# Kernel optimization log

Hardware: AMD Instinct MI355X
Metric: run time of the kernel (lower is better)

The kernel has to match this reference:

```python
import jax, jax.numpy as jnp
import numpy as np

VOCAB, EMB, H, T, B, S = 30000, 300, 512, 9, 128, 256


def setup_inputs() -> dict:
    key = jax.random.key(0)
    ks = jax.random.split(key, 16)
    sc = 0.1
    inp = {
        "inputs": jax.random.randint(ks[0], (B, S), 0, VOCAB, dtype=jnp.int32),
        "tags": jax.random.randint(ks[1], (B, S), 0, T, dtype=jnp.int32),
        "masks": jnp.ones((B, S), dtype=bool),
        "emb": jax.random.normal(ks[2], (VOCAB, EMB), jnp.float32),
        "w_ih_f": jax.random.normal(ks[3], (4 * H, EMB), jnp.float32) * sc,
        "w_hh_f": jax.random.normal(ks[4], (4 * H, H), jnp.float32) * sc,
        "b_f": jax.random.normal(ks[5], (4 * H,), jnp.float32) * sc,
        "w_ih_b": jax.random.normal(ks[6], (4 * H, EMB), jnp.float32) * sc,
        "w_hh_b": jax.random.normal(ks[7], (4 * H, H), jnp.float32) * sc,
        "b_b": jax.random.normal(ks[8], (4 * H,), jnp.float32) * sc,
        "fc_w": jax.random.normal(ks[9], (T, 2 * H), jnp.float32) * sc,
        "trans": jax.random.normal(ks[10], (T, T), jnp.float32) * sc,
        "start_trans": jax.random.normal(ks[11], (T,), jnp.float32) * sc,
        "end_trans": jax.random.normal(ks[12], (T,), jnp.float32) * sc,
    }
    return inp


def _run_lstm(x, w_ih, w_hh, b, reverse):
    # x: (B,S,E); pytorch gate order i,f,g,o; b = b_ih + b_hh combined
    xg = jnp.einsum('bse,ge->bsg', x, w_ih) + b  # (B,S,4H)
    if reverse:
        xg = xg[:, ::-1]
    h0 = jnp.zeros((x.shape[0], w_hh.shape[1]), x.dtype)

    def step(carry, xt):
        h, c = carry
        g = xt + h @ w_hh.T
        i, f, gg, o = jnp.split(g, 4, axis=-1)
        c = jax.nn.sigmoid(f) * c + jax.nn.sigmoid(i) * jnp.tanh(gg)
        h = jax.nn.sigmoid(o) * jnp.tanh(c)
        return (h, c), h

    _, hs = jax.lax.scan(step, (h0, h0), xg.transpose(1, 0, 2))
    hs = hs.transpose(1, 0, 2)  # (B,S,H)
    if reverse:
        hs = hs[:, ::-1]
    return hs


def _crf_llh(emissions, tags, masks, trans, start_trans, end_trans):
    # torchcrf log-likelihood, reduction='sum'
    Bn, Sn, Tn = emissions.shape
    mf = masks.astype(emissions.dtype)
    bidx = jnp.arange(Bn)
    first = tags[:, 0]
    num = start_trans[first] + emissions[bidx, 0, first]
    prev, cur = tags[:, :-1], tags[:, 1:]
    step_sc = trans[prev, cur] + jnp.take_along_axis(emissions[:, 1:], cur[..., None], -1)[..., 0]
    num = num + jnp.sum(step_sc * mf[:, 1:], axis=1)
    seq_ends = masks.sum(1) - 1
    last = tags[bidx, seq_ends]
    num = num + end_trans[last]

    score0 = start_trans + emissions[:, 0]  # (B,T)

    def step(score, xs):
        em_t, m_t = xs  # (B,T), (B,)
        nxt = jax.nn.logsumexp(score[:, :, None] + trans[None] + em_t[:, None, :], axis=1)
        score = jnp.where(m_t[:, None], nxt, score)
        return score, None

    score, _ = jax.lax.scan(step, score0,
                            (emissions[:, 1:].transpose(1, 0, 2), masks[:, 1:].T))
    logZ = jax.nn.logsumexp(score + end_trans, axis=1)
    return jnp.sum(num - logZ)


def reference(inputs, tags, masks, emb, w_ih_f, w_hh_f, b_f, w_ih_b, w_hh_b, b_b,
              fc_w, trans, start_trans, end_trans):
    x = emb[inputs]  # (B,S,E); dropout is identity at eval
    hf = _run_lstm(x, w_ih_f, w_hh_f, b_f, reverse=False)
    hb = _run_lstm(x, w_ih_b, w_hh_b, b_b, reverse=True)
    feats = jnp.concatenate([hf, hb], axis=-1)  # (B,S,2H)
    emissions = jnp.einsum('bsh,th->bst', feats, fc_w)
    return _crf_llh(emissions, tags, masks, trans, start_trans, end_trans)
```

## Files before the change

### kernel.cpp

```cpp
#include <hip/hip_runtime.h>
#include <hip/hip_bf16.h>
#include <stdint.h>

#define B_    128
#define S_    256
#define T_    9

typedef __bf16 bf16;
typedef bf16  bf16x8 __attribute__((ext_vector_type(8)));
typedef bf16  bf16x4 __attribute__((ext_vector_type(4)));
typedef float f32x4  __attribute__((ext_vector_type(4)));
typedef unsigned long long u64;

__device__ __forceinline__ float sigm(float x)  { return 1.f / (1.f + __expf(-x)); }
__device__ __forceinline__ float tanhx(float x) { return 2.f / (1.f + __expf(-2.f * x)) - 1.f; }

#define SBlg() do { asm volatile("s_waitcnt lgkmcnt(0)" ::: "memory"); \
                    __builtin_amdgcn_s_barrier(); } while (0)

__global__ void prep_kernel(const float* __restrict__ wihf, const float* __restrict__ whhf,
                            const float* __restrict__ bf_,  const float* __restrict__ wihb,
                            const float* __restrict__ whhb, const float* __restrict__ bb_,
                            bf16* __restrict__ wih_r, bf16* __restrict__ whh_r,
                            float* __restrict__ bias_r)
{
    int64_t idx = (int64_t)blockIdx.x * blockDim.x + threadIdx.x;
    const int64_t N1 = 2LL * 2048 * 320;
    const int64_t N2 = 2LL * 2048 * 512;
    const int64_t N3 = 4096;
    if (idx < N1) {
        int k = (int)(idx % 320);
        int64_t r = idx / 320;
        int row = (int)(r % 2048), dir = (int)(r / 2048);
        const float* w = dir ? wihb : wihf;
        int orig = (row & 3) * 512 + (row >> 2);
        float v = (k < 300) ? w[(int64_t)orig * 300 + k] : 0.f;
        wih_r[idx] = (bf16)v;
    } else if (idx < N1 + N2) {
        int64_t i = idx - N1;
        int k = (int)(i % 512);
        int64_t r = i / 512;
        int row = (int)(r % 2048), dir = (int)(r / 2048);
        const float* w = dir ? whhb : whhf;
        int orig = (row & 3) * 512 + (row >> 2);
        int x = k & 31;
        int ks = (x & 16) | (((x >> 1) & 1) << 3) | ((x & 1) << 2)
               | (((x >> 3) & 1) << 1) | ((x >> 2) & 1);
        int ksrc = (k & ~31) | ks;
        whh_r[i] = (bf16)w[(int64_t)orig * 512 + ksrc];
    } else if (idx < N1 + N2 + N3) {
        int i = (int)(idx - (N1 + N2));
        int row = i & 2047, dir = i >> 11;
        const float* bb = dir ? bb_ : bf_;
        int orig = (row & 3) * 512 + (row >> 2);
        bias_r[i] = bb[orig];
    }
}

__global__ __launch_bounds__(256, 1) void fused_lstm_kernel(
    const int* __restrict__ inputs, const float* __restrict__ emb,
    const bf16* __restrict__ wih_r, const bf16* __restrict__ whh_r,
    const float* __restrict__ bias_r, const float* __restrict__ fcw,
    u64* __restrict__ hbuf, float* __restrict__ em_part)
{
    const int bid = blockIdx.x;
    const int gid = bid & 15;
    const int gslice = bid >> 4;
    const int dir = gid >> 3, bs = gid & 7;
    const int tid = threadIdx.x;
    const int w = tid >> 6, lane = tid & 63;
    const int l15 = lane & 15, l4 = lane >> 4;

    __shared__ __align__(16) char h_s[16384];
    __shared__ __align__(16) char ring[16384];
    __shared__ __align__(16) char x_s[20480];
    __shared__ __align__(16) bf16 h_sm[2 * 16 * 32];
    __shared__ float em_lds[2][2][144];

    auto load_h = [&](int t) {
        const u64 wt = (u64)t;
        const u64 want = (wt << 16) | (wt << 48);
        const u64 MSK  = 0xffff0000ffff0000ull;
        const u64* base = hbuf + ((size_t)(((t & 1) * 2 + dir) * 8 + bs) * 16) * 256 + tid;
        const u64* p0 = base;        const u64* p1 = base + 512;
        const u64* p2 = base + 1024; const u64* p3 = base + 1536;
        const u64* p4 = base + 2048; const u64* p5 = base + 2560;
        const u64* p6 = base + 3072; const u64* p7 = base + 3584;
        u64 v[16];
        asm volatile(
            "global_load_dwordx2 %0, %16, off sc1\n\t"
            "global_load_dwordx2 %1, %16, off offset:2048 sc1\n\t"
            "global_load_dwordx2 %2, %17, off sc1\n\t"
            "global_load_dwordx2 %3, %17, off offset:2048 sc1\n\t"
            "global_load_dwordx2 %4, %18, off sc1\n\t"
            "global_load_dwordx2 %5, %18, off offset:2048 sc1\n\t"
            "global_load_dwordx2 %6, %19, off sc1\n\t"
            "global_load_dwordx2 %7, %19, off offset:2048 sc1\n\t"
            "global_load_dwordx2 %8, %20, off sc1\n\t"
            "global_load_dwordx2 %9, %20, off offset:2048 sc1\n\t"
            "global_load_dwordx2 %10, %21, off sc1\n\t"
            "global_load_dwordx2 %11, %21, off offset:2048 sc1\n\t"
            "global_load_dwordx2 %12, %22, off sc1\n\t"
            "global_load_dwordx2 %13, %22, off offset:2048 sc1\n\t"
            "global_load_dwordx2 %14, %23, off sc1\n\t"
            "global_load_dwordx2 %15, %23, off offset:2048 sc1\n\t"
            "s_waitcnt vmcnt(0)"
            : "=&v"(v[0]), "=&v"(v[1]), "=&v"(v[2]), "=&v"(v[3]),
              "=&v"(v[4]), "=&v"(v[5]), "=&v"(v[6]), "=&v"(v[7]),
              "=&v"(v[8]), "=&v"(v[9]), "=&v"(v[10]), "=&v"(v[11]),
              "=&v"(v[12]), "=&v"(v[13]), "=&v"(v[14]), "=&v"(v[15])
            : "v"(p0), "v"(p1), "v"(p2), "v"(p3),
              "v"(p4), "v"(p5), "v"(p6), "v"(p7)
            : "memory");
        __builtin_amdgcn_sched_barrier(0);
        int rounds = 0;
        while (true) {
            unsigned wst = 0;
#pragma unroll
            for (int g = 0; g < 16; ++g)
                if (__any((int)((v[g] & MSK) != want))) wst |= (1u << g);
            if (wst == 0) break;
            if (++rounds > (1 << 14)) break;
            if (rounds > 1) __builtin_amdgcn_s_sleep(1);
#pragma unroll
            for (int g = 0; g < 16; ++g)
                if (wst & (1u << g))
                    asm volatile("global_load_dwordx2 %0, %1, off sc1"
                                 : "=v"(v[g]) : "v"(base + g * 256) : "memory");
            asm volatile("s_waitcnt vmcnt(0)" ::: "memory");
            __builtin_amdgcn_sched_barrier(0);
        }
        const int b = tid >> 4, k0 = (tid & 15) * 2;
#pragma unroll
        for (int g = 0; g < 16; ++g) {
            unsigned two = (unsigned)(v[g] & 0xffff) | ((unsigned)((v[g] >> 32) & 0xffff) << 16);
            *(unsigned*)(h_s + (((b * 512 + g * 32 + k0) * 2) ^ ((b & 7) << 4))) = two;
        }
    };

    if (w < 2) {
        bf16x8 aw[4][16];
        {
            const int64_t wrow0 = (int64_t)(dir * 2048 + gslice * 128 + w * 64);
#pragma unroll
            for (int tile = 0; tile < 4; ++tile)
#pragma unroll
                for (int kt = 0; kt < 16; ++kt)
                    aw[tile][kt] = *(const bf16x8*)(whh_r + (wrow0 + tile * 16 + l15) * 512 + kt * 32 + l4 * 8);
        }
        float c[4] = {0.f, 0.f, 0.f, 0.f};
        SBlg();
        SBlg();
        for (int t = 0; t < 256; ++t) {
            const int pp = t & 1;
            load_h(t);
            SBlg();
            f32x4 acc[4];
#pragma unroll
            for (int tile = 0; tile < 4; ++tile) {
                int g = w * 64 + tile * 16 + l4 * 4;
                acc[tile] = *(const f32x4*)(ring + pp * 8192 + ((l15 * 512 + g * 4) ^ ((l15 & 7) << 4)));
            }
#pragma unroll
            for (int kt = 0; kt < 16; ++kt) {
                bf16x8 hf = *(const bf16x8*)(h_s + (((l15 * 512 + kt * 32 + l4 * 8) * 2) ^ ((l15 & 7) << 4)));
#pragma unroll
                for (int tile = 0; tile < 4; ++tile)
                    acc[tile] = __builtin_amdgcn_mfma_f32_16x16x32_bf16(aw[tile][kt], hf, acc[tile], 0, 0, 0);
            }
            bf16x4 hv;
#pragma unroll
            for (int tile = 0; tile < 4; ++tile) {
                float ig = sigm(acc[tile][0]), fg = sigm(acc[tile][1]);
                float gg = tanhx(acc[tile][2]), og = sigm(acc[tile][3]);
                c[tile] = fg * c[tile] + ig * gg;
                float h = og * tanhx(c[tile]);
                hv[tile] = (bf16)h;
            }
            if (t < 255) {
                const u64 tg = (u64)(t + 1);
                const u64 tag2 = (tg << 16) | (tg << 48);
                u64 hb;
                __builtin_memcpy(&hb, &hv, 8);
                u64 d0 = (hb & 0xffff) | (((hb >> 16) & 0xffff) << 32) | tag2;
                u64 d1 = ((hb >> 32) & 0xffff) | (((hb >> 48) & 0xffff) << 32) | tag2;
                u64* dst = hbuf
                    + ((size_t)((((t + 1) & 1) * 2 + dir) * 8 + bs) * 16 + gslice) * 256
                    + l15 * 16 + w * 8 + l4 * 2;
                __hip_atomic_store(dst,     d0, __ATOMIC_RELAXED, __HIP_MEMORY_SCOPE_AGENT);
                __hip_atomic_store(dst + 1, d1, __ATOMIC_RELAXED, __HIP_MEMORY_SCOPE_AGENT);
            }
#pragma unroll
            for (int tile = 0; tile < 4; ++tile)
                h_sm[pp * 512 + l15 * 32 + (w * 16 + tile * 4 + l4)] = hv[tile];
            SBlg();
        }
        SBlg();
    } else {
        const int w2 = w - 2;
        bf16x8 ap[4][10];
        f32x4 bias_v[4];
        {
            const int64_t prow0 = (int64_t)(dir * 2048 + gslice * 128 + w2 * 64);
#pragma unroll
            for (int tile = 0; tile < 4; ++tile) {
#pragma unroll
                for (int kt = 0; kt < 10; ++kt)
                    ap[tile][kt] = *(const bf16x8*)(wih_r + (prow0 + tile * 16 + l15) * 320 + kt * 32 + l4 * 8);
                bias_v[tile] = *(const f32x4*)(bias_r + prow0 + tile * 16 + l4 * 4);
            }
        }
        const int hdl = w2 * 16 + l4 * 4;
        float fcv[4][9];
#pragma unroll
        for (int j = 0; j < 4; ++j)
#pragma unroll
            for (int tg = 0; tg < 9; ++tg)
                fcv[j][tg] = fcw[tg * 1024 + dir * 512 + gslice * 32 + hdl + j];

        auto stage_x = [&](int slot, int tx) {
            int j = w2 * 8 + (lane >> 3);
            int cb = (lane & 7) * 40;
            int tok = inputs[(bs * 16 + j) * 256 + tx];
            const float* er = emb + (int64_t)tok * 300;
#pragma unroll
            for (int i = 0; i < 10; ++i) {
                int col = cb + i * 4;
                float4 vv = make_float4(0.f, 0.f, 0.f, 0.f);
                if (col < 300) vv = *(const float4*)(er + col);
                bf16x4 bv;
                bv[0] = (bf16)vv.x; bv[1] = (bf16)vv.y; bv[2] = (bf16)vv.z; bv[3] = (bf16)vv.w;
                *(bf16x4*)(x_s + slot * 10240 + ((j * 640 + col * 2) ^ ((j & 7) << 4))) = bv;
            }
        };
        auto ring_compute = [&](int xslot, int rslot) {
            f32x4 accp[4];
#pragma unroll
            for (int tile = 0; tile < 4; ++tile) accp[tile] = bias_v[tile];
#pragma unroll
            for (int kt = 0; kt < 10; ++kt) {
                bf16x8 xf = *(const bf16x8*)(x_s + xslot * 10240 + ((l15 * 640 + (kt * 32 + l4 * 8) * 2) ^ ((l15 & 7) << 4)));
#pragma unroll
                for (int tile = 0; tile < 4; ++tile)
                    accp[tile] = __builtin_amdgcn_mfma_f32_16x16x32_bf16(ap[tile][kt], xf, accp[tile], 0, 0, 0);
            }
#pragma unroll
            for (int tile = 0; tile < 4; ++tile) {
                int g = w2 * 64 + tile * 16 + l4 * 4;
                *(f32x4*)(ring + rslot * 8192 + ((l15 * 512 + g * 4) ^ ((l15 & 7) << 4))) = accp[tile];
            }
        };
        auto emis_accum = [&](int slot) {
            bf16x4 hv4 = *(const bf16x4*)(h_sm + slot * 512 + l15 * 32 + hdl);
            float h0 = (float)hv4[0], h1 = (float)hv4[1], h2 = (float)hv4[2], h3 = (float)hv4[3];
#pragma unroll
            for (int tg = 0; tg < 9; ++tg) {
                float p = h0 * fcv[0][tg] + h1 * fcv[1][tg] + h2 * fcv[2][tg] + h3 * fcv[3][tg];
                p += __shfl_xor(p, 16);
                p += __shfl_xor(p, 32);
                if (l4 == 0) em_lds[w2][slot][tg * 16 + l15] = p;
            }
        };
        auto consume = [&](int slot, int tx) {
            int idx = w2 * 64 + lane;
            {
                int tg = idx >> 4, bl = idx & 15;
                float vv = em_lds[0][slot][idx] + em_lds[1][slot][idx];
                atomicAdd(em_part + (((int64_t)gslice * 128 + bs * 16 + bl) * 256 + tx) * 9 + tg, vv);
            }
            if (w2 == 0 && lane < 16) {
                int idx2 = 128 + lane;
                int tg = idx2 >> 4, bl = idx2 & 15;
                float vv = em_lds[0][slot][idx2] + em_lds[1][slot][idx2];
                atomicAdd(em_part + (((int64_t)gslice * 128 + bs * 16 + bl) * 256 + tx) * 9 + tg, vv);
            }
        };

        stage_x(0, dir ? 255 : 0);
        stage_x(1, dir ? 254 : 1);
        SBlg();
        ring_compute(0, 0);
        SBlg();
        for (int t = 0; t < 256; ++t) {
            load_h(t);
            SBlg();
            if (t < 255) ring_compute((t + 1) & 1, (t + 1) & 1);
            if (t >= 1) emis_accum((t - 1) & 1);
            if (t >= 2) consume((t - 2) & 1, dir ? 255 - (t - 2) : t - 2);
            if (t <= 253) stage_x(t & 1, dir ? 255 - (t + 2) : t + 2);
            SBlg();
        }
        emis_accum(1);
        consume(0, dir ? 1 : 254);
        SBlg();
        consume(1, dir ? 0 : 255);
    }
}

__global__ __launch_bounds__(256) void reduce_em_kernel(const float* __restrict__ part,
                                                        float* __restrict__ em)
{
    int idx = blockIdx.x * 256 + threadIdx.x;
    if (idx >= 128 * 256 * 9) return;
    float s = 0.f;
#pragma unroll
    for (int g = 0; g < 16; ++g) s += part[(int64_t)g * (128 * 256 * 9) + idx];
    em[idx] = s;
}

__global__ __launch_bounds__(64) void crf_kernel(const float* __restrict__ em,
                                                 const int* __restrict__ tags,
                                                 const float* __restrict__ trans,
                                                 const float* __restrict__ strans,
                                                 const float* __restrict__ etrans,
                                                 float* __restrict__ partial)
{
    const int b = blockIdx.x;
    const int lane = threadIdx.x;
    const int* tg = tags + b * 256;
    const float* eb = em + (int64_t)b * 256 * 9;

    float ns = 0.f;
    for (int t = lane; t < 256; t += 64) {
        int cur = tg[t];
        float v = eb[t * 9 + cur];
        v += (t == 0) ? strans[cur] : trans[tg[t - 1] * 9 + cur];
        ns += v;
    }
#pragma unroll
    for (int o = 32; o; o >>= 1) ns += __shfl_xor(ns, o);
    float num = ns + etrans[tg[255]];

    int j = lane < 9 ? lane : 8;
    float trow[9];
#pragma unroll
    for (int i = 0; i < 9; ++i) trow[i] = trans[i * 9 + j];
    float sc = strans[j] + eb[j];
    for (int t = 1; t < 256; ++t) {
        float e = eb[t * 9 + j];
        float m = -1e30f;
        float s[9];
#pragma unroll
        for (int i = 0; i < 9; ++i) {
            s[i] = __shfl(sc, i) + trow[i];
            m = fmaxf(m, s[i]);
        }
        float sum = 0.f;
#pragma unroll
        for (int i = 0; i < 9; ++i) sum += __expf(s[i] - m);
        sc = m + __logf(sum) + e;
    }
    float z = (lane < 9) ? (sc + etrans[lane]) : -1e30f;
    float zm = z;
#pragma unroll
    for (int o = 32; o; o >>= 1) zm = fmaxf(zm, __shfl_xor(zm, o));
    float zs = __expf(z - zm);
#pragma unroll
    for (int o = 32; o; o >>= 1) zs += __shfl_xor(zs, o);
    float logZ = zm + __logf(zs);
    if (lane == 0) partial[b] = num - logZ;
}

__global__ void reduce_kernel(const float* __restrict__ partial, float* __restrict__ out)
{
    int l = threadIdx.x;
    float v = partial[l];
#pragma unroll
    for (int o = 32; o; o >>= 1) v += __shfl_xor(v, o);
    __shared__ float s2[2];
    if ((l & 63) == 0) s2[l >> 6] = v;
    __syncthreads();
    if (l == 0) out[0] = s2[0] + s2[1];
}

extern "C" void kernel_launch(void* const* d_in, const int* in_sizes, int n_in,
                              void* d_out, int out_size, void* d_ws, size_t ws_size,
                              hipStream_t stream)
{
    char* ws = (char*)d_ws;
    size_t off = 0;
    auto alloc = [&](size_t bytes) -> char* {
        char* p = ws + off;
        off += (bytes + 255) & ~(size_t)255;
        return p;
    };
    bf16*  wih_r  = (bf16*) alloc((size_t)4096 * 320 * 2);
    bf16*  whh_r  = (bf16*) alloc((size_t)2 * 2048 * 512 * 2);
    float* bias_r = (float*)alloc((size_t)4096 * 4);
    u64*   hbuf   = (u64*)  alloc((size_t)32 * 16 * 256 * 8);
    float* em_part= (float*)alloc((size_t)16 * 128 * 256 * 9 * 4);
    float* em     = (float*)alloc((size_t)128 * 256 * 9 * 4);
    float* partial= (float*)alloc((size_t)128 * 4);
    const size_t NEEDED = off;

    float* out = (float*)d_out;
    if (ws_size < NEEDED) {
        hipMemsetAsync(out, 0, sizeof(float) * (size_t)out_size, stream);
        return;
    }

    const int*   inputs = (const int*)  d_in[0];
    const int*   tags   = (const int*)  d_in[1];
    const float* emb    = (const float*)d_in[3];
    const float* wihf   = (const float*)d_in[4];
    const float* whhf   = (const float*)d_in[5];
    const float* bfv    = (const float*)d_in[6];
    const float* wihb   = (const float*)d_in[7];
    const float* whhb   = (const float*)d_in[8];
    const float* bbv    = (const float*)d_in[9];
    const float* fcw    = (const float*)d_in[10];
    const float* trans  = (const float*)d_in[11];
    const float* strans = (const float*)d_in[12];
    const float* etrans = (const float*)d_in[13];

    hipMemsetAsync(hbuf, 0, (size_t)32 * 16 * 256 * 8, stream);
    hipMemsetAsync(em_part, 0, (size_t)16 * 128 * 256 * 9 * 4, stream);

    {
        int64_t N = 2LL * 2048 * 320 + 2LL * 2048 * 512 + 4096;
        int blocks = (int)((N + 255) / 256);
        prep_kernel<<<blocks, 256, 0, stream>>>(wihf, whhf, bfv, wihb, whhb, bbv, wih_r, whh_r, bias_r);
    }
    fused_lstm_kernel<<<256, 256, 0, stream>>>(inputs, emb, wih_r, whh_r, bias_r, fcw,
                                               hbuf, em_part);
    reduce_em_kernel<<<(128 * 256 * 9 + 255) / 256, 256, 0, stream>>>(em_part, em);
    crf_kernel<<<128, 64, 0, stream>>>(em, tags, trans, strans, etrans, partial);
    reduce_kernel<<<1, 128, 0, stream>>>(partial, out);
}
```

Before: 1.151 ms.

## Interleave two batch chunks per block to hide cross-block recurrence latency

Each block now handles two batch chunks, alternating their recurrent steps, so the grid drops from 256 to 128 blocks. While one chunk waits on global h exchange from the other blocks, the other chunk's MFMA work can proceed, which is meant to hide the inter-block sync latency. LDS buffers for ring, x, h and emissions are doubled per chunk. The cost is more serial work per block and a doubled LDS footprint, on half as many CUs.

```diff
diff --git a/kernel.cpp b/kernel.cpp
--- a/kernel.cpp
+++ b/kernel.cpp
@@ -64,20 +64,23 @@
     u64* __restrict__ hbuf, float* __restrict__ em_part)
 {
     const int bid = blockIdx.x;
-    const int gid = bid & 15;
-    const int gslice = bid >> 4;
-    const int dir = gid >> 3, bs = gid & 7;
+    const int gslice = bid >> 3;
+    const int g8 = bid & 7;
+    const int dir = g8 >> 2, bsq = g8 & 3;
     const int tid = threadIdx.x;
     const int w = tid >> 6, lane = tid & 63;
     const int l15 = lane & 15, l4 = lane >> 4;
 
     __shared__ __align__(16) char h_s[16384];
-    __shared__ __align__(16) char ring[16384];
-    __shared__ __align__(16) char x_s[20480];
-    __shared__ __align__(16) bf16 h_sm[2 * 16 * 32];
-    __shared__ float em_lds[2][2][144];
-
-    auto load_h = [&](int t) {
+    __shared__ __align__(16) char ring[2][2][8192];
+    __shared__ __align__(16) char x_s[2][2][10240];
+    __shared__ __align__(16) bf16 h_sm[2][2][512];
+    __shared__ float em_lds[2][2][2][144];
+
+    auto txOf = [&](int q) { return dir ? 255 - q : q; };
+
+    auto load_h = [&](int c01, int t) {
+        const int bs = bsq + c01 * 4;
         const u64 wt = (u64)t;
         const u64 want = (wt << 16) | (wt << 48);
         const u64 MSK  = 0xffff0000ffff0000ull;
@@ -148,18 +151,20 @@
                 for (int kt = 0; kt < 16; ++kt)
                     aw[tile][kt] = *(const bf16x8*)(whh_r + (wrow0 + tile * 16 + l15) * 512 + kt * 32 + l4 * 8);
         }
-        float c[4] = {0.f, 0.f, 0.f, 0.f};
-        SBlg();
-        SBlg();
-        for (int t = 0; t < 256; ++t) {
+        float cA[4] = {0.f, 0.f, 0.f, 0.f}, cB[4] = {0.f, 0.f, 0.f, 0.f};
+        SBlg();
+        SBlg();
+
+        auto recPhase = [&](int c01, int t, float (&c)[4]) {
             const int pp = t & 1;
-            load_h(t);
+            const int bs = bsq + c01 * 4;
+            load_h(c01, t);
             SBlg();
             f32x4 acc[4];
 #pragma unroll
             for (int tile = 0; tile < 4; ++tile) {
                 int g = w * 64 + tile * 16 + l4 * 4;
-                acc[tile] = *(const f32x4*)(ring + pp * 8192 + ((l15 * 512 + g * 4) ^ ((l15 & 7) << 4)));
+                acc[tile] = *(const f32x4*)(ring[c01][pp] + ((l15 * 512 + g * 4) ^ ((l15 & 7) << 4)));
             }
 #pragma unroll
             for (int kt = 0; kt < 16; ++kt) {
@@ -192,8 +197,13 @@
             }
 #pragma unroll
             for (int tile = 0; tile < 4; ++tile)
-                h_sm[pp * 512 + l15 * 32 + (w * 16 + tile * 4 + l4)] = hv[tile];
+                h_sm[c01][pp][l15 * 32 + (w * 16 + tile * 4 + l4)] = hv[tile];
             SBlg();
+        };
+
+        for (int t = 0; t < 256; ++t) {
+            recPhase(0, t, cA);
+            recPhase(1, t, cB);
         }
         SBlg();
     } else {
@@ -218,7 +228,8 @@
             for (int tg = 0; tg < 9; ++tg)
                 fcv[j][tg] = fcw[tg * 1024 + dir * 512 + gslice * 32 + hdl + j];
 
-        auto stage_x = [&](int slot, int tx) {
+        auto stage_x = [&](int c01, int slot, int tx) {
+            const int bs = bsq + c01 * 4;
             int j = w2 * 8 + (lane >> 3);
             int cb = (lane & 7) * 40;
             int tok = inputs[(bs * 16 + j) * 256 + tx];
@@ -230,16 +241,16 @@
                 if (col < 300) vv = *(const float4*)(er + col);
                 bf16x4 bv;
                 bv[0] = (bf16)vv.x; bv[1] = (bf16)vv.y; bv[2] = (bf16)vv.z; bv[3] = (bf16)vv.w;
-                *(bf16x4*)(x_s + slot * 10240 + ((j * 640 + col * 2) ^ ((j & 7) << 4))) = bv;
-            }
-        };
-        auto ring_compute = [&](int xslot, int rslot) {
+                *(bf16x4*)(x_s[c01][slot] + ((j * 640 + col * 2) ^ ((j & 7) << 4))) = bv;
+            }
+        };
+        auto ring_compute = [&](int c01, int slot) {
             f32x4 accp[4];
 #pragma unroll
             for (int tile = 0; tile < 4; ++tile) accp[tile] = bias_v[tile];
 #pragma unroll
             for (int kt = 0; kt < 10; ++kt) {
-                bf16x8 xf = *(const bf16x8*)(x_s + xslot * 10240 + ((l15 * 640 + (kt * 32 + l4 * 8) * 2) ^ ((l15 & 7) << 4)));
+                bf16x8 xf = *(const bf16x8*)(x_s[c01][slot] + ((l15 * 640 + (kt * 32 + l4 * 8) * 2) ^ ((l15 & 7) << 4)));
 #pragma unroll
                 for (int tile = 0; tile < 4; ++tile)
                     accp[tile] = __builtin_amdgcn_mfma_f32_16x16x32_bf16(ap[tile][kt], xf, accp[tile], 0, 0, 0);
@@ -247,53 +258,61 @@
 #pragma unroll
             for (int tile = 0; tile < 4; ++tile) {
                 int g = w2 * 64 + tile * 16 + l4 * 4;
-                *(f32x4*)(ring + rslot * 8192 + ((l15 * 512 + g * 4) ^ ((l15 & 7) << 4))) = accp[tile];
-            }
-        };
-        auto emis_accum = [&](int slot) {
-            bf16x4 hv4 = *(const bf16x4*)(h_sm + slot * 512 + l15 * 32 + hdl);
+                *(f32x4*)(ring[c01][slot] + ((l15 * 512 + g * 4) ^ ((l15 & 7) << 4))) = accp[tile];
+            }
+        };
+        auto emis_accum = [&](int c01, int slot) {
+            bf16x4 hv4 = *(const bf16x4*)&h_sm[c01][slot][l15 * 32 + hdl];
             float h0 = (float)hv4[0], h1 = (float)hv4[1], h2 = (float)hv4[2], h3 = (float)hv4[3];
 #pragma unroll
             for (int tg = 0; tg < 9; ++tg) {
                 float p = h0 * fcv[0][tg] + h1 * fcv[1][tg] + h2 * fcv[2][tg] + h3 * fcv[3][tg];
                 p += __shfl_xor(p, 16);
                 p += __shfl_xor(p, 32);
-                if (l4 == 0) em_lds[w2][slot][tg * 16 + l15] = p;
-            }
-        };
-        auto consume = [&](int slot, int tx) {
+                if (l4 == 0) em_lds[w2][c01][slot][tg * 16 + l15] = p;
+            }
+        };
+        auto consume = [&](int c01, int slot, int tx) {
+            const int bs = bsq + c01 * 4;
             int idx = w2 * 64 + lane;
             {
                 int tg = idx >> 4, bl = idx & 15;
-                float vv = em_lds[0][slot][idx] + em_lds[1][slot][idx];
+                float vv = em_lds[0][c01][slot][idx] + em_lds[1][c01][slot][idx];
                 atomicAdd(em_part + (((int64_t)gslice * 128 + bs * 16 + bl) * 256 + tx) * 9 + tg, vv);
             }
             if (w2 == 0 && lane < 16) {
                 int idx2 = 128 + lane;
                 int tg = idx2 >> 4, bl = idx2 & 15;
-                float vv = em_lds[0][slot][idx2] + em_lds[1][slot][idx2];
+                float vv = em_lds[0][c01][slot][idx2] + em_lds[1][c01][slot][idx2];
                 atomicAdd(em_part + (((int64_t)gslice * 128 + bs * 16 + bl) * 256 + tx) * 9 + tg, vv);
             }
         };
 
-        stage_x(0, dir ? 255 : 0);
-        stage_x(1, dir ? 254 : 1);
+        stage_x(0, 0, txOf(0)); stage_x(0, 1, txOf(1));
+        stage_x(1, 0, txOf(0)); stage_x(1, 1, txOf(1));
         SBlg();
         ring_compute(0, 0);
-        SBlg();
+        ring_compute(1, 0);
+        SBlg();
+
+        auto projPhase = [&](int c01, int t) {
+            load_h(c01, t);
+            SBlg();
+            if (t < 255) ring_compute(c01, (t + 1) & 1);
+            if (t >= 1)  emis_accum(c01, (t - 1) & 1);
+            if (t >= 2)  consume(c01, (t - 2) & 1, txOf(t - 2));
+            if (t <= 253) stage_x(c01, t & 1, txOf(t + 2));
+            SBlg();
+        };
+
         for (int t = 0; t < 256; ++t) {
-            load_h(t);
-            SBlg();
-            if (t < 255) ring_compute((t + 1) & 1, (t + 1) & 1);
-            if (t >= 1) emis_accum((t - 1) & 1);
-            if (t >= 2) consume((t - 2) & 1, dir ? 255 - (t - 2) : t - 2);
-            if (t <= 253) stage_x(t & 1, dir ? 255 - (t + 2) : t + 2);
-            SBlg();
-        }
-        emis_accum(1);
-        consume(0, dir ? 1 : 254);
-        SBlg();
-        consume(1, dir ? 0 : 255);
+            projPhase(0, t);
+            projPhase(1, t);
+        }
+        emis_accum(0, 1); emis_accum(1, 1);
+        consume(0, 0, txOf(254)); consume(1, 0, txOf(254));
+        SBlg();
+        consume(0, 1, txOf(255)); consume(1, 1, txOf(255));
     }
 }
 
@@ -421,7 +440,7 @@
         int blocks = (int)((N + 255) / 256);
         prep_kernel<<<blocks, 256, 0, stream>>>(wihf, whhf, bfv, wihb, whhb, bbv, wih_r, whh_r, bias_r);
     }
-    fused_lstm_kernel<<<256, 256, 0, stream>>>(inputs, emb, wih_r, whh_r, bias_r, fcw,
+    fused_lstm_kernel<<<128, 256, 0, stream>>>(inputs, emb, wih_r, whh_r, bias_r, fcw,
                                                hbuf, em_part);
     reduce_em_kernel<<<(128 * 256 * 9 + 255) / 256, 256, 0, stream>>>(em_part, em);
     crf_kernel<<<128, 64, 0, stream>>>(em, tags, trans, strans, etrans, partial);
```

Measured after the change: 2.225 ms. +93.3%, slower.
